# Optimization experiments

Measured on AMD Instinct MI355X. Metric: run time of the kernel, lower is better.

Reference implementation:

```python
import jax, jax.numpy as jnp
import numpy as np

N_NODES = 50000
N_EDGES = 800000
IN_CH = 128
HID = 64
MLP_HID = 128
EPS = 1e-5


def setup_inputs() -> dict:
    key = jax.random.key(0)
    ks = iter(jax.random.split(key, 32))
    d = {}
    d['x'] = jax.random.normal(next(ks), (N_NODES, IN_CH), dtype=jnp.float32)
    d['edge_index'] = jax.random.randint(next(ks), (2, N_EDGES), 0, N_NODES, dtype=jnp.int64)

    def lin(k, out_c, in_c, scale=None):
        s = scale if scale is not None else 1.0 / np.sqrt(in_c)
        return jax.random.uniform(k, (out_c, in_c), jnp.float32, -s, s)

    # layer 0: in->hid, with residual linear
    d['Wl0'] = lin(next(ks), HID, IN_CH); d['bl0'] = jnp.zeros((HID,), jnp.float32)
    d['Wr0'] = lin(next(ks), HID, IN_CH)
    d['g0'] = jnp.ones((HID,), jnp.float32); d['be0'] = jnp.zeros((HID,), jnp.float32)
    d['rW0'] = lin(next(ks), HID, IN_CH); d['rb0'] = jnp.zeros((HID,), jnp.float32)
    # layers 1,2: hid->hid, identity residual
    for i in (1, 2):
        d[f'Wl{i}'] = lin(next(ks), HID, HID); d[f'bl{i}'] = jnp.zeros((HID,), jnp.float32)
        d[f'Wr{i}'] = lin(next(ks), HID, HID)
        d[f'g{i}'] = jnp.ones((HID,), jnp.float32); d[f'be{i}'] = jnp.zeros((HID,), jnp.float32)
    # edge MLP: 2*HID -> MLP_HID -> MLP_HID -> 1
    d['W1'] = lin(next(ks), MLP_HID, 2 * HID); d['b1'] = jnp.zeros((MLP_HID,), jnp.float32)
    d['W2'] = lin(next(ks), MLP_HID, MLP_HID); d['b2'] = jnp.zeros((MLP_HID,), jnp.float32)
    d['W3'] = lin(next(ks), 1, MLP_HID); d['b3'] = jnp.zeros((1,), jnp.float32)
    return d


def _res_sage_layer(x, src, tgt, Wl, bl, Wr, g, be, rW=None, rb=None):
    # SAGEConv (mean aggr): out = lin_l(mean_{j in N(i)} x_j) + lin_r(x_i)
    msg = x[src]                                              # [E, C] gather
    agg = jax.ops.segment_sum(msg, tgt, num_segments=N_NODES)
    cnt = jax.ops.segment_sum(jnp.ones((msg.shape[0],), x.dtype), tgt, num_segments=N_NODES)
    mean = agg / jnp.maximum(cnt, 1.0)[:, None]
    out = mean @ Wl.T + bl + x @ Wr.T
    # BatchNorm (training-mode batch statistics, biased var)
    mu = out.mean(axis=0)
    var = out.var(axis=0)
    out = (out - mu) * jax.lax.rsqrt(var + EPS) * g + be
    out = jax.nn.relu(out)
    res = x @ rW.T + rb if rW is not None else x
    return out + res


def reference(x, edge_index, Wl0, bl0, Wr0, g0, be0, rW0, rb0,
              Wl1, bl1, Wr1, g1, be1, Wl2, bl2, Wr2, g2, be2,
              W1, b1, W2, b2, W3, b3):
    src, tgt = edge_index[0], edge_index[1]
    h = _res_sage_layer(x, src, tgt, Wl0, bl0, Wr0, g0, be0, rW0, rb0)
    h = _res_sage_layer(h, src, tgt, Wl1, bl1, Wr1, g1, be1)
    h = _res_sage_layer(h, src, tgt, Wl2, bl2, Wr2, g2, be2)
    edge_repr = jnp.concatenate([h[src], h[tgt]], axis=1)     # [E, 2*HID]
    z = jax.nn.relu(edge_repr @ W1.T + b1)                    # dropout: eval mode (identity)
    z = jax.nn.relu(z @ W2.T + b2)
    return z @ W3.T + b3                                      # [E, 1]
```

## Files before the change

### kernel.cpp

```cpp
#include <hip/hip_runtime.h>
#include <hip/hip_bf16.h>

#define NN 50000
#define NE 800000
#define HID 64
#define EPSV 1e-5f
#define NBLK 196

typedef __attribute__((ext_vector_type(8))) short bf16x8;
typedef __attribute__((ext_vector_type(4))) float f32x4;
typedef __attribute__((ext_vector_type(4))) int int4v;

__device__ __forceinline__ ushort f2b(float f) {
    union { __hip_bfloat16 b; ushort u; } c;
    c.b = __float2bfloat16(f);
    return c.u;
}
__device__ __forceinline__ float b2f(ushort u) {
    return __uint_as_float(((unsigned int)u) << 16);
}

__global__ void prep_all_kernel(
    const float* __restrict__ W1, const float* __restrict__ W2,
    const float* __restrict__ Wl0, const float* __restrict__ Wr0, const float* __restrict__ rW0,
    const float* __restrict__ Wl1, const float* __restrict__ Wr1,
    const float* __restrict__ Wl2, const float* __restrict__ Wr2,
    ushort* __restrict__ W1b, ushort* __restrict__ W2b,
    ushort* __restrict__ wnb, int* __restrict__ icnt, float* __restrict__ bnbuf)
{
    int i = blockIdx.x * 256 + threadIdx.x;
    if      (i < 16384)  W1b[i] = f2b(W1[i]);
    else if (i < 32768)  W2b[i - 16384] = f2b(W2[i - 16384]);
    else if (i < 40960)  wnb[i - 32768] = f2b(Wl0[i - 32768]);
    else if (i < 49152)  wnb[i - 32768] = f2b(Wr0[i - 40960]);
    else if (i < 57344)  wnb[i - 32768] = f2b(rW0[i - 49152]);
    else if (i < 61440)  wnb[i - 32768] = f2b(Wl1[i - 57344]);
    else if (i < 65536)  wnb[i - 32768] = f2b(Wr1[i - 61440]);
    else if (i < 69632)  wnb[i - 32768] = f2b(Wl2[i - 65536]);
    else if (i < 73728)  wnb[i - 32768] = f2b(Wr2[i - 69632]);
    else if (i < 123728) icnt[i - 73728] = 0;
    else if (i < 124112) bnbuf[i - 123728] = 0.f;
}

__global__ void count_kernel(const int* __restrict__ tgt, int* __restrict__ icnt) {
    int e = blockIdx.x * 256 + threadIdx.x;
    if (e < NE) atomicAdd(&icnt[tgt[e]], 1);
}

__global__ void scanA_kernel(const int* __restrict__ icnt, int* __restrict__ off,
                             int* __restrict__ bsum) {
    __shared__ int s[256];
    const int t = threadIdx.x;
    const int i = blockIdx.x * 256 + t;
    int v = (i < NN) ? icnt[i] : 0;
    s[t] = v;
    __syncthreads();
    for (int d = 1; d < 256; d <<= 1) {
        int x = (t >= d) ? s[t - d] : 0;
        __syncthreads();
        s[t] += x;
        __syncthreads();
    }
    if (i < NN) off[i] = s[t];
    if (t == 255) bsum[blockIdx.x] = s[255];
}

__global__ void scanB_kernel(const int* __restrict__ icnt, const int* __restrict__ bsum,
                             int* __restrict__ off, int* __restrict__ woff) {
    __shared__ int red[256];
    const int t = threadIdx.x, bid = blockIdx.x;
    int s = 0;
    for (int j = t; j < bid; j += 256) s += bsum[j];
    red[t] = s;
    __syncthreads();
    for (int d = 128; d > 0; d >>= 1) {
        if (t < d) red[t] += red[t + d];
        __syncthreads();
    }
    const int bpre = red[0];
    const int i = bid * 256 + t;
    if (i < NN) {
        int e = off[i] - icnt[i] + bpre;
        off[i] = e;
        woff[i] = e;
        if (i == NN - 1) off[NN] = NE;
    }
}

__global__ void fill_kernel(const int* __restrict__ src, const int* __restrict__ tgt,
                            int* __restrict__ woff, int* __restrict__ ebuf) {
    int e = blockIdx.x * 256 + threadIdx.x;
    if (e < NE) {
        int p = atomicAdd(&woff[tgt[e]], 1);
        ebuf[p] = src[e];
    }
}

__global__ __launch_bounds__(256) void proj0_mfma_kernel(
    const float* __restrict__ x,
    const ushort* __restrict__ w0, const ushort* __restrict__ w1,
    const ushort* __restrict__ w2,
    const float* __restrict__ bias1, const float* __restrict__ bias2,
    ushort* __restrict__ xb, float* __restrict__ pre, float* __restrict__ res)
{
    __shared__ float sC[128][65];
    const int tid = threadIdx.x;
    const int wv = tid >> 6, lane = tid & 63;
    const int l15 = lane & 15, l4 = lane >> 4;
    const int seg = blockIdx.y;
    const ushort* W = (seg == 0) ? w0 : ((seg == 1) ? w1 : w2);
    const int n0 = blockIdx.x * 128;

    bf16x8 wf[4][4];
    #pragma unroll
    for (int n = 0; n < 4; n++)
        #pragma unroll
        for (int ks = 0; ks < 4; ks++)
            wf[n][ks] = *(const bf16x8*)&W[(n * 16 + l15) * 128 + ks * 32 + l4 * 8];

    f32x4 acc[2][4];
    #pragma unroll
    for (int m = 0; m < 2; m++)
        #pragma unroll
        for (int n = 0; n < 4; n++)
            acc[m][n] = (f32x4){0.f, 0.f, 0.f, 0.f};

    #pragma unroll
    for (int m = 0; m < 2; m++) {
        int row = n0 + wv * 32 + m * 16 + l15;
        if (row > NN - 1) row = NN - 1;
        #pragma unroll
        for (int ks = 0; ks < 4; ks++) {
            const float* ap = &x[(long)row * 128 + ks * 32 + l4 * 8];
            float4 f0 = *(const float4*)ap;
            float4 f1 = *(const float4*)(ap + 4);
            union { ushort u[8]; bf16x8 b; } a;
            a.u[0] = f2b(f0.x); a.u[1] = f2b(f0.y); a.u[2] = f2b(f0.z); a.u[3] = f2b(f0.w);
            a.u[4] = f2b(f1.x); a.u[5] = f2b(f1.y); a.u[6] = f2b(f1.z); a.u[7] = f2b(f1.w);
            #pragma unroll
            for (int n = 0; n < 4; n++)
                acc[m][n] = __builtin_amdgcn_mfma_f32_16x16x32_bf16(a.b, wf[n][ks], acc[m][n], 0, 0, 0);
        }
    }
    #pragma unroll
    for (int m = 0; m < 2; m++)
        #pragma unroll
        for (int n = 0; n < 4; n++)
            #pragma unroll
            for (int r = 0; r < 4; r++)
                sC[wv * 32 + m * 16 + l4 * 4 + r][n * 16 + l15] = acc[m][n][r];
    __syncthreads();

    const int r = tid >> 1, ch = (tid & 1) * 32;
    const int node = n0 + r;
    if (node < NN) {
        if (seg == 0) {
            #pragma unroll
            for (int g = 0; g < 4; g++) {
                union { ushort u[8]; int4v v; } pk;
                #pragma unroll
                for (int j = 0; j < 8; j++)
                    pk.u[j] = f2b(sC[r][ch + g * 8 + j]);
                *(int4v*)&xb[(long)node * 64 + ch + g * 8] = pk.v;
            }
        } else {
            float* O = (seg == 1) ? pre : res;
            const float* bp = (seg == 1) ? bias1 : bias2;
            #pragma unroll
            for (int g = 0; g < 8; g++) {
                int c = ch + g * 4;
                float4 v = make_float4(sC[r][c + 0] + bp[c + 0], sC[r][c + 1] + bp[c + 1],
                                       sC[r][c + 2] + bp[c + 2], sC[r][c + 3] + bp[c + 3]);
                *(float4*)&O[(long)node * 64 + c] = v;
            }
        }
    }
}

__global__ __launch_bounds__(256) void gather_bn_kernel(
    const int* __restrict__ off, const int* __restrict__ ebuf,
    const ushort* __restrict__ xb,
    float* __restrict__ vbase,
    float* __restrict__ bnsum, float* __restrict__ bnsq)
{
    __shared__ float r1[4][64], r2[4][64];
    const int lane = threadIdx.x & 63;
    const int wid = __builtin_amdgcn_readfirstlane(threadIdx.x >> 6);
    const int eslot = lane >> 3;
    const int cg = lane & 7;
    float s8[8], q8[8];
    #pragma unroll
    for (int j = 0; j < 8; j++) { s8[j] = 0.f; q8[j] = 0.f; }

    for (int n = blockIdx.x * 4 + wid; n < NN; n += gridDim.x * 4) {
        const int a = off[n], b = off[n + 1];
        float acc[8];
        #pragma unroll
        for (int j = 0; j < 8; j++) acc[j] = 0.f;
        for (int p = a + eslot; p < b; p += 8) {
            int sidx = ebuf[p];
            union { int4v v; ushort u[8]; } cv;
            cv.v = *(const int4v*)&xb[(long)sidx * 64 + cg * 8];
            #pragma unroll
            for (int j = 0; j < 8; j++) acc[j] += b2f(cv.u[j]);
        }
        #pragma unroll
        for (int m = 8; m <= 32; m <<= 1)
            #pragma unroll
            for (int j = 0; j < 8; j++)
                acc[j] += __shfl_xor(acc[j], m);
        if (eslot == 0) {
            const float inv_deg = 1.0f / fmaxf((float)(b - a), 1.f);
            float4 p0 = *(const float4*)&vbase[(long)n * 64 + cg * 8];
            float4 p1 = *(const float4*)&vbase[(long)n * 64 + cg * 8 + 4];
            float v[8];
            v[0] = acc[0] * inv_deg + p0.x; v[1] = acc[1] * inv_deg + p0.y;
            v[2] = acc[2] * inv_deg + p0.z; v[3] = acc[3] * inv_deg + p0.w;
            v[4] = acc[4] * inv_deg + p1.x; v[5] = acc[5] * inv_deg + p1.y;
            v[6] = acc[6] * inv_deg + p1.z; v[7] = acc[7] * inv_deg + p1.w;
            *(float4*)&vbase[(long)n * 64 + cg * 8]     = make_float4(v[0], v[1], v[2], v[3]);
            *(float4*)&vbase[(long)n * 64 + cg * 8 + 4] = make_float4(v[4], v[5], v[6], v[7]);
            #pragma unroll
            for (int j = 0; j < 8; j++) { s8[j] += v[j]; q8[j] += v[j] * v[j]; }
        }
    }
    if (eslot == 0) {
        #pragma unroll
        for (int j = 0; j < 8; j++) {
            r1[wid][cg * 8 + j] = s8[j];
            r2[wid][cg * 8 + j] = q8[j];
        }
    }
    __syncthreads();
    if (threadIdx.x < 64) {
        float s = r1[0][lane] + r1[1][lane] + r1[2][lane] + r1[3][lane];
        float q = r2[0][lane] + r2[1][lane] + r2[2][lane] + r2[3][lane];
        atomicAdd(&bnsum[lane], s);
        atomicAdd(&bnsq[lane], q);
    }
}

__global__ __launch_bounds__(256) void apply_proj_kernel(
    const float* __restrict__ vIn,
    const float* __restrict__ resb,
    const float* __restrict__ bnsum, const float* __restrict__ bnsq,
    const float* __restrict__ g, const float* __restrict__ be,
    float* __restrict__ hout,
    const ushort* __restrict__ Wl, const ushort* __restrict__ Wr,
    const float* __restrict__ bias,
    ushort* __restrict__ xb, float* __restrict__ preOut)
{
    __shared__ float scs[64], shs[64];
    __shared__ ushort tile[128 * 72];
    __shared__ float sC[128][65];
    const int tid = threadIdx.x;
    const int n0 = blockIdx.x * 128;
    const int wv = tid >> 6, lane = tid & 63;
    const int l15 = lane & 15, l4 = lane >> 4;

    if (tid < 64) {
        const float inv_n = 1.0f / (float)NN;
        float mu = bnsum[tid] * inv_n;
        float var = bnsq[tid] * inv_n - mu * mu;
        float rstd = rsqrtf(var + EPSV);
        float sc = g[tid] * rstd;
        scs[tid] = sc;
        shs[tid] = be[tid] - mu * sc;
    }
    __syncthreads();

    {
        const int rloc = tid >> 1;
        const int n = n0 + rloc;
        const int ch = (tid & 1) * 32;
        if (n < NN) {
            #pragma unroll
            for (int gq = 0; gq < 4; gq++) {
                int c = ch + gq * 8;
                float4 v0 = *(const float4*)&vIn[(long)n * 64 + c];
                float4 v1 = *(const float4*)&vIn[(long)n * 64 + c + 4];
                float4 r0 = *(const float4*)&resb[(long)n * 64 + c];
                float4 r1 = *(const float4*)&resb[(long)n * 64 + c + 4];
                float o[8];
                o[0] = fmaxf(fmaf(v0.x, scs[c + 0], shs[c + 0]), 0.f) + r0.x;
                o[1] = fmaxf(fmaf(v0.y, scs[c + 1], shs[c + 1]), 0.f) + r0.y;
                o[2] = fmaxf(fmaf(v0.z, scs[c + 2], shs[c + 2]), 0.f) + r0.z;
                o[3] = fmaxf(fmaf(v0.w, scs[c + 3], shs[c + 3]), 0.f) + r0.w;
                o[4] = fmaxf(fmaf(v1.x, scs[c + 4], shs[c + 4]), 0.f) + r1.x;
                o[5] = fmaxf(fmaf(v1.y, scs[c + 5], shs[c + 5]), 0.f) + r1.y;
                o[6] = fmaxf(fmaf(v1.z, scs[c + 6], shs[c + 6]), 0.f) + r1.z;
                o[7] = fmaxf(fmaf(v1.w, scs[c + 7], shs[c + 7]), 0.f) + r1.w;
                *(float4*)&hout[(long)n * 64 + c]     = make_float4(o[0], o[1], o[2], o[3]);
                *(float4*)&hout[(long)n * 64 + c + 4] = make_float4(o[4], o[5], o[6], o[7]);
                union { ushort u[8]; int4v v; } pk;
                #pragma unroll
                for (int j = 0; j < 8; j++) pk.u[j] = f2b(o[j]);
                int byte = rloc * 144 + ((c * 2) ^ ((rloc & 7) << 4));
                *(int4v*)((char*)tile + byte) = pk.v;
            }
        }
    }
    __syncthreads();

    for (int seg = 0; seg < 2; seg++) {
        const ushort* W = seg ? Wr : Wl;
        bf16x8 wf[4][2];
        #pragma unroll
        for (int n = 0; n < 4; n++)
            #pragma unroll
            for (int ks = 0; ks < 2; ks++)
                wf[n][ks] = *(const bf16x8*)&W[(n * 16 + l15) * 64 + ks * 32 + l4 * 8];

        f32x4 acc[2][4];
        #pragma unroll
        for (int m = 0; m < 2; m++)
            #pragma unroll
            for (int n = 0; n < 4; n++)
                acc[m][n] = (f32x4){0.f, 0.f, 0.f, 0.f};

        #pragma unroll
        for (int m = 0; m < 2; m++) {
            const int row = wv * 32 + m * 16 + l15;
            #pragma unroll
            for (int ks = 0; ks < 2; ks++) {
                int byte = row * 144 + ((((ks * 32 + l4 * 8) * 2)) ^ ((row & 7) << 4));
                bf16x8 a = *(const bf16x8*)((const char*)tile + byte);
                #pragma unroll
                for (int n = 0; n < 4; n++)
                    acc[m][n] = __builtin_amdgcn_mfma_f32_16x16x32_bf16(a, wf[n][ks], acc[m][n], 0, 0, 0);
            }
        }
        #pragma unroll
        for (int m = 0; m < 2; m++)
            #pragma unroll
            for (int n = 0; n < 4; n++)
                #pragma unroll
                for (int r = 0; r < 4; r++)
                    sC[wv * 32 + m * 16 + l4 * 4 + r][n * 16 + l15] = acc[m][n][r];
        __syncthreads();

        const int r = tid >> 1, ch = (tid & 1) * 32;
        const int node = n0 + r;
        if (node < NN) {
            if (seg == 0) {
                #pragma unroll
                for (int gq = 0; gq < 4; gq++) {
                    union { ushort u[8]; int4v v; } pk;
                    #pragma unroll
                    for (int j = 0; j < 8; j++)
                        pk.u[j] = f2b(sC[r][ch + gq * 8 + j]);
                    *(int4v*)&xb[(long)node * 64 + ch + gq * 8] = pk.v;
                }
            } else {
                #pragma unroll
                for (int gq = 0; gq < 8; gq++) {
                    int c = ch + gq * 4;
                    float4 v = make_float4(sC[r][c + 0] + bias[c + 0], sC[r][c + 1] + bias[c + 1],
                                           sC[r][c + 2] + bias[c + 2], sC[r][c + 3] + bias[c + 3]);
                    *(float4*)&preOut[(long)node * 64 + c] = v;
                }
            }
        }
        __syncthreads();
    }
}

__global__ void apply_final_kernel(const float* __restrict__ vIn,
                                   const float* __restrict__ resb,
                                   const float* __restrict__ bnsum, const float* __restrict__ bnsq,
                                   const float* __restrict__ g, const float* __restrict__ be,
                                   ushort* __restrict__ hb)
{
    const float inv_n = 1.0f / (float)NN;
    const int stride = gridDim.x * 256;
    for (int i = blockIdx.x * 256 + threadIdx.x; i < NN * 16; i += stride) {
        int n = i >> 4;
        int c0 = (i & 15) * 4;
        float sc[4], sh[4];
        #pragma unroll
        for (int j = 0; j < 4; j++) {
            int c = c0 + j;
            float mu = bnsum[c] * inv_n;
            float var = bnsq[c] * inv_n - mu * mu;
            float rstd = rsqrtf(var + EPSV);
            sc[j] = g[c] * rstd;
            sh[j] = be[c] - mu * sc[j];
        }
        float4 v = *(const float4*)&vIn[(long)n * 64 + c0];
        float4 r = *(const float4*)&resb[(long)n * 64 + c0];
        union { ushort u[4]; uint2 v2; } p;
        p.u[0] = f2b(fmaxf(fmaf(v.x, sc[0], sh[0]), 0.f) + r.x);
        p.u[1] = f2b(fmaxf(fmaf(v.y, sc[1], sh[1]), 0.f) + r.y);
        p.u[2] = f2b(fmaxf(fmaf(v.z, sc[2], sh[2]), 0.f) + r.z);
        p.u[3] = f2b(fmaxf(fmaf(v.w, sc[3], sh[3]), 0.f) + r.w);
        *(uint2*)&hb[(long)n * 64 + c0] = p.v2;
    }
}

#define NSTRIP 25000
#define EMG 256
#define ZSTR 136

#define GATHER(ss)                                                        \
    do {                                                                  \
        int e0g = (ss) * 32;                                              \
        _Pragma("unroll")                                                 \
        for (int m = 0; m < 2; m++) {                                     \
            int e = e0g + m * 16 + l15;                                   \
            const ushort* hs = hb + (long)src[e] * 64;                    \
            const ushort* ht = hb + (long)tgt[e] * 64;                    \
            ga[m][0] = *(const bf16x8*)&hs[l4 * 8];                       \
            ga[m][1] = *(const bf16x8*)&hs[32 + l4 * 8];                  \
            ga[m][2] = *(const bf16x8*)&ht[l4 * 8];                       \
            ga[m][3] = *(const bf16x8*)&ht[32 + l4 * 8];                  \
        }                                                                 \
    } while (0)

__global__ __launch_bounds__(512) void edge_mlp_wave_kernel(
    const ushort* __restrict__ hb,
    const int* __restrict__ src, const int* __restrict__ tgt,
    const ushort* __restrict__ W1b, const ushort* __restrict__ W2b,
    const float* __restrict__ b1, const float* __restrict__ b2,
    const float* __restrict__ W3, const float* __restrict__ b3,
    float* __restrict__ out)
{
    __shared__ ushort wlds[32768];
    __shared__ ushort z1[8][32 * ZSTR];

    const int tid = threadIdx.x;
    const int wid = tid >> 6, lane = tid & 63;
    const int l15 = lane & 15, l4 = lane >> 4;

    for (int c = tid; c < 4096; c += 512) {
        int layer = c >> 11, oc = (c >> 4) & 127, kc = c & 15;
        const ushort* Wsrc = layer ? W2b : W1b;
        int4v v = *(const int4v*)&Wsrc[oc * 128 + kc * 8];
        int byte = layer * 32768 + oc * 256 + ((kc * 16) ^ ((oc & 7) << 4));
        *(int4v*)((char*)wlds + byte) = v;
    }

    float b1v[8], b2v[8], w3v[8];
    #pragma unroll
    for (int n = 0; n < 8; n++) {
        int oc = n * 16 + l15;
        b1v[n] = b1[oc]; b2v[n] = b2[oc]; w3v[n] = W3[oc];
    }
    const float b3v = b3[0];

    const int bid = blockIdx.x;
    const int q = NSTRIP / EMG, r = NSTRIP % EMG;
    const int t0 = bid * q + (bid < r ? bid : r);
    const int nt = q + (bid < r ? 1 : 0);
    ushort* zw = z1[wid];

    bf16x8 ga[2][4];
    if (wid < nt) GATHER(t0 + wid);
    __syncthreads();

    for (int j = wid; j < nt; j += 8) {
        const int e0 = (t0 + j) * 32;

        f32x4 acc[2][8];
        #pragma unroll
        for (int m = 0; m < 2; m++)
            #pragma unroll
            for (int n = 0; n < 8; n++)
                acc[m][n] = (f32x4){b1v[n], b1v[n], b1v[n], b1v[n]};
        #pragma unroll
        for (int ks = 0; ks < 4; ks++) {
            bf16x8 wf[8];
            #pragma unroll
            for (int n = 0; n < 8; n++) {
                int oc = n * 16 + l15;
                int byte = oc * 256 + (((ks * 4 + l4) * 16) ^ ((oc & 7) << 4));
                wf[n] = *(const bf16x8*)((const char*)wlds + byte);
            }
            #pragma unroll
            for (int m = 0; m < 2; m++)
                #pragma unroll
                for (int n = 0; n < 8; n++)
                    acc[m][n] = __builtin_amdgcn_mfma_f32_16x16x32_bf16(ga[m][ks], wf[n], acc[m][n], 0, 0, 0);
        }
        #pragma unroll
        for (int m = 0; m < 2; m++)
            #pragma unroll
            for (int n = 0; n < 8; n++) {
                int col = n * 16 + l15;
                #pragma unroll
                for (int rr = 0; rr < 4; rr++)
                    zw[(m * 16 + l4 * 4 + rr) * ZSTR + col] = f2b(fmaxf(acc[m][n][rr], 0.f));
            }

        if (j + 8 < nt) GATHER(t0 + j + 8);

        f32x4 acc2[2][8];
        #pragma unroll
        for (int m = 0; m < 2; m++)
            #pragma unroll
            for (int n = 0; n < 8; n++)
                acc2[m][n] = (f32x4){b2v[n], b2v[n], b2v[n], b2v[n]};
        #pragma unroll
        for (int ks = 0; ks < 4; ks++) {
            bf16x8 wf[8];
            #pragma unroll
            for (int n = 0; n < 8; n++) {
                int oc = n * 16 + l15;
                int byte = 32768 + oc * 256 + (((ks * 4 + l4) * 16) ^ ((oc & 7) << 4));
                wf[n] = *(const bf16x8*)((const char*)wlds + byte);
            }
            bf16x8 a2[2];
            #pragma unroll
            for (int m = 0; m < 2; m++)
                a2[m] = *(const bf16x8*)&zw[(m * 16 + l15) * ZSTR + ks * 32 + l4 * 8];
            #pragma unroll
            for (int m = 0; m < 2; m++)
                #pragma unroll
                for (int n = 0; n < 8; n++)
                    acc2[m][n] = __builtin_amdgcn_mfma_f32_16x16x32_bf16(a2[m], wf[n], acc2[m][n], 0, 0, 0);
        }

        #pragma unroll
        for (int m = 0; m < 2; m++) {
            float sv[4];
            #pragma unroll
            for (int rr = 0; rr < 4; rr++) {
                float s = 0.f;
                #pragma unroll
                for (int n = 0; n < 8; n++)
                    s = fmaf(fmaxf(acc2[m][n][rr], 0.f), w3v[n], s);
                s += __shfl_xor(s, 1);
                s += __shfl_xor(s, 2);
                s += __shfl_xor(s, 4);
                s += __shfl_xor(s, 8);
                sv[rr] = s + b3v;
            }
            if (l15 == 0)
                *(float4*)&out[e0 + m * 16 + l4 * 4] =
                    make_float4(sv[0], sv[1], sv[2], sv[3]);
        }
    }
}

extern "C" void kernel_launch(void* const* d_in, const int* in_sizes, int n_in,
                              void* d_out, int out_size, void* d_ws, size_t ws_size,
                              hipStream_t stream)
{
    const float* x   = (const float*)d_in[0];
    const int*   ei  = (const int*)d_in[1];
    const int* src = ei;
    const int* tgt = ei + NE;
    const float* Wl0 = (const float*)d_in[2];
    const float* bl0 = (const float*)d_in[3];
    const float* Wr0 = (const float*)d_in[4];
    const float* g0  = (const float*)d_in[5];
    const float* be0 = (const float*)d_in[6];
    const float* rW0 = (const float*)d_in[7];
    const float* rb0 = (const float*)d_in[8];
    const float* Wl1 = (const float*)d_in[9];
    const float* bl1 = (const float*)d_in[10];
    const float* Wr1 = (const float*)d_in[11];
    const float* g1  = (const float*)d_in[12];
    const float* be1 = (const float*)d_in[13];
    const float* Wl2 = (const float*)d_in[14];
    const float* bl2 = (const float*)d_in[15];
    const float* Wr2 = (const float*)d_in[16];
    const float* g2  = (const float*)d_in[17];
    const float* be2 = (const float*)d_in[18];
    const float* W1  = (const float*)d_in[19];
    const float* b1  = (const float*)d_in[20];
    const float* W2  = (const float*)d_in[21];
    const float* b2  = (const float*)d_in[22];
    const float* W3  = (const float*)d_in[23];
    const float* b3  = (const float*)d_in[24];
    float* out = (float*)d_out;

    float* ws = (float*)d_ws;
    float*  pre  = ws;
    float*  res  = ws + 3200000;
    float*  hbuf = ws + 6400000;
    ushort* xb   = (ushort*)(ws + 9600256);
    ushort* hb   = (ushort*)(ws + 11200256);
    ushort* W1b  = (ushort*)(ws + 12800256);
    ushort* W2b  = W1b + 16384;
    int*    icnt = (int*)(ws + 12816640);
    int*    off  = icnt + 50000;
    int*    woff = off + 50001;
    int*    ebuf = woff + 50000;
    int*    bsum = ebuf + 800000;
    ushort* wnb  = (ushort*)(ws + 13766912);
    ushort* Wl0b = wnb;
    ushort* Wr0b = wnb + 8192;
    ushort* rW0b = wnb + 16384;
    ushort* Wl1b = wnb + 24576;
    ushort* Wr1b = wnb + 28672;
    ushort* Wl2b = wnb + 32768;
    ushort* Wr2b = wnb + 36864;
    float*  bn   = ws + 13787392;
    float*  bnsum0 = bn,       *bnsq0 = bn + 64;
    float*  bnsum1 = bn + 128, *bnsq1 = bn + 192;
    float*  bnsum2 = bn + 256, *bnsq2 = bn + 320;

    prep_all_kernel<<<485, 256, 0, stream>>>(W1, W2, Wl0, Wr0, rW0, Wl1, Wr1, Wl2, Wr2,
                                             W1b, W2b, wnb, icnt, bn);
    count_kernel<<<NE / 256, 256, 0, stream>>>(tgt, icnt);
    scanA_kernel<<<NBLK, 256, 0, stream>>>(icnt, off, bsum);
    scanB_kernel<<<NBLK, 256, 0, stream>>>(icnt, bsum, off, woff);
    fill_kernel<<<NE / 256, 256, 0, stream>>>(src, tgt, woff, ebuf);

    dim3 g0g(391, 3);
    proj0_mfma_kernel<<<g0g, 256, 0, stream>>>(x, Wl0b, Wr0b, rW0b, bl0, rb0, xb, pre, res);
    gather_bn_kernel<<<1024, 256, 0, stream>>>(off, ebuf, xb, pre, bnsum0, bnsq0);

    apply_proj_kernel<<<391, 256, 0, stream>>>(pre, res, bnsum0, bnsq0, g0, be0,
                                               hbuf, Wl1b, Wr1b, bl1, xb, pre);
    gather_bn_kernel<<<1024, 256, 0, stream>>>(off, ebuf, xb, pre, bnsum1, bnsq1);

    apply_proj_kernel<<<391, 256, 0, stream>>>(pre, hbuf, bnsum1, bnsq1, g1, be1,
                                               hbuf, Wl2b, Wr2b, bl2, xb, pre);
    gather_bn_kernel<<<1024, 256, 0, stream>>>(off, ebuf, xb, pre, bnsum2, bnsq2);

    apply_final_kernel<<<1024, 256, 0, stream>>>(pre, hbuf, bnsum2, bnsq2, g2, be2, hb);

    edge_mlp_wave_kernel<<<EMG, 512, 0, stream>>>(hb, src, tgt, W1b, W2b, b1, b2, W3, b3, out);
}
```

Baseline: 397.1 us.

## Load x tile once into LDS for all three projections; transpose edge-MLP MFMA output

The layer-0 projection kernel used to launch three grid slices that each re-read and re-converted the same fp32 x rows. Now one block loads its 128-row tile once into a swizzled bf16 LDS buffer and loops over the three weight matrices, so x is read from global memory a third as often. The cost is fewer blocks (391 instead of 1173), more LDS per block and extra barriers. Separately, the first edge-MLP MFMA swaps its operands so each lane holds four consecutive output channels, which lets it write the ReLU'd bf16 result to LDS as one 8-byte store instead of four scalar stores, with the bias loaded as a float4.

```diff
diff --git a/kernel.cpp b/kernel.cpp
--- a/kernel.cpp
+++ b/kernel.cpp
@@ -103,77 +103,93 @@
     const float* __restrict__ bias1, const float* __restrict__ bias2,
     ushort* __restrict__ xb, float* __restrict__ pre, float* __restrict__ res)
 {
+    __shared__ ushort xt[128 * 128];
     __shared__ float sC[128][65];
     const int tid = threadIdx.x;
     const int wv = tid >> 6, lane = tid & 63;
     const int l15 = lane & 15, l4 = lane >> 4;
-    const int seg = blockIdx.y;
-    const ushort* W = (seg == 0) ? w0 : ((seg == 1) ? w1 : w2);
     const int n0 = blockIdx.x * 128;
 
-    bf16x8 wf[4][4];
-    #pragma unroll
-    for (int n = 0; n < 4; n++)
-        #pragma unroll
-        for (int ks = 0; ks < 4; ks++)
-            wf[n][ks] = *(const bf16x8*)&W[(n * 16 + l15) * 128 + ks * 32 + l4 * 8];
-
-    f32x4 acc[2][4];
-    #pragma unroll
-    for (int m = 0; m < 2; m++)
-        #pragma unroll
-        for (int n = 0; n < 4; n++)
-            acc[m][n] = (f32x4){0.f, 0.f, 0.f, 0.f};
-
-    #pragma unroll
-    for (int m = 0; m < 2; m++) {
-        int row = n0 + wv * 32 + m * 16 + l15;
-        if (row > NN - 1) row = NN - 1;
-        #pragma unroll
-        for (int ks = 0; ks < 4; ks++) {
-            const float* ap = &x[(long)row * 128 + ks * 32 + l4 * 8];
-            float4 f0 = *(const float4*)ap;
-            float4 f1 = *(const float4*)(ap + 4);
-            union { ushort u[8]; bf16x8 b; } a;
+    {
+        const int rloc = tid >> 1;
+        int row = n0 + rloc; if (row > NN - 1) row = NN - 1;
+        const int c0 = (tid & 1) * 64;
+        #pragma unroll
+        for (int gq = 0; gq < 8; gq++) {
+            int c = c0 + gq * 8;
+            float4 f0 = *(const float4*)&x[(long)row * 128 + c];
+            float4 f1 = *(const float4*)&x[(long)row * 128 + c + 4];
+            union { ushort u[8]; int4v v; } a;
             a.u[0] = f2b(f0.x); a.u[1] = f2b(f0.y); a.u[2] = f2b(f0.z); a.u[3] = f2b(f0.w);
             a.u[4] = f2b(f1.x); a.u[5] = f2b(f1.y); a.u[6] = f2b(f1.z); a.u[7] = f2b(f1.w);
+            int byte = rloc * 256 + ((c * 2) ^ ((rloc & 7) << 4));
+            *(int4v*)((char*)xt + byte) = a.v;
+        }
+    }
+    __syncthreads();
+
+    for (int seg = 0; seg < 3; seg++) {
+        const ushort* W = (seg == 0) ? w0 : ((seg == 1) ? w1 : w2);
+        bf16x8 wf[4][4];
+        #pragma unroll
+        for (int n = 0; n < 4; n++)
+            #pragma unroll
+            for (int ks = 0; ks < 4; ks++)
+                wf[n][ks] = *(const bf16x8*)&W[(n * 16 + l15) * 128 + ks * 32 + l4 * 8];
+
+        f32x4 acc[2][4];
+        #pragma unroll
+        for (int m = 0; m < 2; m++)
             #pragma unroll
             for (int n = 0; n < 4; n++)
-                acc[m][n] = __builtin_amdgcn_mfma_f32_16x16x32_bf16(a.b, wf[n][ks], acc[m][n], 0, 0, 0);
-        }
-    }
-    #pragma unroll
-    for (int m = 0; m < 2; m++)
-        #pragma unroll
-        for (int n = 0; n < 4; n++)
-            #pragma unroll
-            for (int r = 0; r < 4; r++)
-                sC[wv * 32 + m * 16 + l4 * 4 + r][n * 16 + l15] = acc[m][n][r];
-    __syncthreads();
-
-    const int r = tid >> 1, ch = (tid & 1) * 32;
-    const int node = n0 + r;
-    if (node < NN) {
-        if (seg == 0) {
-            #pragma unroll
-            for (int g = 0; g < 4; g++) {
-                union { ushort u[8]; int4v v; } pk;
-                #pragma unroll
-                for (int j = 0; j < 8; j++)
-                    pk.u[j] = f2b(sC[r][ch + g * 8 + j]);
-                *(int4v*)&xb[(long)node * 64 + ch + g * 8] = pk.v;
-            }
-        } else {
-            float* O = (seg == 1) ? pre : res;
-            const float* bp = (seg == 1) ? bias1 : bias2;
-            #pragma unroll
-            for (int g = 0; g < 8; g++) {
-                int c = ch + g * 4;
-                float4 v = make_float4(sC[r][c + 0] + bp[c + 0], sC[r][c + 1] + bp[c + 1],
-                                       sC[r][c + 2] + bp[c + 2], sC[r][c + 3] + bp[c + 3]);
-                *(float4*)&O[(long)node * 64 + c] = v;
-            }
-        }
+                acc[m][n] = (f32x4){0.f, 0.f, 0.f, 0.f};
+
+        #pragma unroll
+        for (int m = 0; m < 2; m++) {
+            const int row = wv * 32 + m * 16 + l15;
+            #pragma unroll
+            for (int ks = 0; ks < 4; ks++) {
+                int byte = row * 256 + ((ks * 64 + l4 * 16) ^ ((row & 7) << 4));
+                bf16x8 a = *(const bf16x8*)((const char*)xt + byte);
+                #pragma unroll
+                for (int n = 0; n < 4; n++)
+                    acc[m][n] = __builtin_amdgcn_mfma_f32_16x16x32_bf16(a, wf[n][ks], acc[m][n], 0, 0, 0);
+            }
+        }
+        #pragma unroll
+        for (int m = 0; m < 2; m++)
+            #pragma unroll
+            for (int n = 0; n < 4; n++)
+                #pragma unroll
+                for (int r = 0; r < 4; r++)
+                    sC[wv * 32 + m * 16 + l4 * 4 + r][n * 16 + l15] = acc[m][n][r];
+        __syncthreads();
+
+        const int r = tid >> 1, ch = (tid & 1) * 32;
+        const int node = n0 + r;
+        if (node < NN) {
+            if (seg == 0) {
+                #pragma unroll
+                for (int gq = 0; gq < 4; gq++) {
+                    union { ushort u[8]; int4v v; } pk;
+                    #pragma unroll
+                    for (int j = 0; j < 8; j++)
+                        pk.u[j] = f2b(sC[r][ch + gq * 8 + j]);
+                    *(int4v*)&xb[(long)node * 64 + ch + gq * 8] = pk.v;
+                }
+            } else {
+                float* O = (seg == 1) ? pre : res;
+                const float* bp = (seg == 1) ? bias1 : bias2;
+                #pragma unroll
+                for (int gq = 0; gq < 8; gq++) {
+                    int c = ch + gq * 4;
+                    float4 v = make_float4(sC[r][c + 0] + bp[c + 0], sC[r][c + 1] + bp[c + 1],
+                                           sC[r][c + 2] + bp[c + 2], sC[r][c + 3] + bp[c + 3]);
+                    *(float4*)&O[(long)node * 64 + c] = v;
+                }
+            }
+        }
+        __syncthreads();
     }
 }
 
@@ -439,11 +455,13 @@
         *(int4v*)((char*)wlds + byte) = v;
     }
 
-    float b1v[8], b2v[8], w3v[8];
+    float4 b1q[8];
+    float b2v[8], w3v[8];
     #pragma unroll
     for (int n = 0; n < 8; n++) {
+        b1q[n] = *(const float4*)&b1[n * 16 + l4 * 4];
         int oc = n * 16 + l15;
-        b1v[n] = b1[oc]; b2v[n] = b2[oc]; w3v[n] = W3[oc];
+        b2v[n] = b2[oc]; w3v[n] = W3[oc];
     }
     const float b3v = b3[0];
 
@@ -465,7 +483,7 @@
         for (int m = 0; m < 2; m++)
             #pragma unroll
             for (int n = 0; n < 8; n++)
-                acc[m][n] = (f32x4){b1v[n], b1v[n], b1v[n], b1v[n]};
+                acc[m][n] = (f32x4){b1q[n].x, b1q[n].y, b1q[n].z, b1q[n].w};
         #pragma unroll
         for (int ks = 0; ks < 4; ks++) {
             bf16x8 wf[8];
@@ -479,16 +497,17 @@
             for (int m = 0; m < 2; m++)
                 #pragma unroll
                 for (int n = 0; n < 8; n++)
-                    acc[m][n] = __builtin_amdgcn_mfma_f32_16x16x32_bf16(ga[m][ks], wf[n], acc[m][n], 0, 0, 0);
+                    acc[m][n] = __builtin_amdgcn_mfma_f32_16x16x32_bf16(wf[n], ga[m][ks], acc[m][n], 0, 0, 0);
         }
         #pragma unroll
         for (int m = 0; m < 2; m++)
             #pragma unroll
             for (int n = 0; n < 8; n++) {
-                int col = n * 16 + l15;
+                union { ushort u[4]; uint2 d; } pk;
                 #pragma unroll
                 for (int rr = 0; rr < 4; rr++)
-                    zw[(m * 16 + l4 * 4 + rr) * ZSTR + col] = f2b(fmaxf(acc[m][n][rr], 0.f));
+                    pk.u[rr] = f2b(fmaxf(acc[m][n][rr], 0.f));
+                *(uint2*)&zw[(m * 16 + l15) * ZSTR + n * 16 + l4 * 4] = pk.d;
             }
 
         if (j + 8 < nt) GATHER(t0 + j + 8);
@@ -607,8 +626,7 @@
     scanB_kernel<<<NBLK, 256, 0, stream>>>(icnt, bsum, off, woff);
     fill_kernel<<<NE / 256, 256, 0, stream>>>(src, tgt, woff, ebuf);
 
-    dim3 g0g(391, 3);
-    proj0_mfma_kernel<<<g0g, 256, 0, stream>>>(x, Wl0b, Wr0b, rW0b, bl0, rb0, xb, pre, res);
+    proj0_mfma_kernel<<<391, 256, 0, stream>>>(x, Wl0b, Wr0b, rW0b, bl0, rb0, xb, pre, res);
     gather_bn_kernel<<<1024, 256, 0, stream>>>(off, ebuf, xb, pre, bnsum0, bnsq0);
 
     apply_proj_kernel<<<391, 256, 0, stream>>>(pre, res, bnsum0, bnsq0, g0, be0,
```

New measurement: 389.0 us. 2.0% less time.
